# Kernel optimization log

Measured on AMD Instinct MI355X. Metric: run time of the kernel, lower is better.

Reference implementation:

```python
import jax, jax.numpy as jnp
import numpy as np

N_NODES = 50000
N_EDGES = 800000
IN_DIM = 128
HID = 32
HEADS = 4
OUT_DIM = 64
NEG_SLOPE = 0.2


def _glorot(key, shape):
    fan = shape[0] + shape[-1] if len(shape) > 1 else shape[-1]
    lim = jnp.sqrt(6.0 / fan)
    return jax.random.uniform(key, shape, jnp.float32, -lim, lim)


def setup_inputs() -> dict:
    key = jax.random.key(0)
    ks = jax.random.split(key, 10)
    x = jax.random.normal(ks[0], (N_NODES, IN_DIM), jnp.float32)
    edge_index = jax.random.randint(ks[1], (2, N_EDGES), 0, N_NODES, jnp.int32)
    # layer 1: in=IN_DIM, heads=HEADS, out=HID, concat
    W1 = _glorot(ks[2], (IN_DIM, HEADS * HID))
    a_src1 = _glorot(ks[3], (HEADS, HID))
    a_dst1 = _glorot(ks[4], (HEADS, HID))
    b1 = jnp.zeros((HEADS * HID,), jnp.float32)
    # layer 2: in=HEADS*HID, heads=1, out=OUT_DIM, mean
    W2 = _glorot(ks[5], (HEADS * HID, OUT_DIM))
    a_src2 = _glorot(ks[6], (1, OUT_DIM))
    a_dst2 = _glorot(ks[7], (1, OUT_DIM))
    b2 = jnp.zeros((OUT_DIM,), jnp.float32)
    return {"x": x, "edge_index": edge_index, "W1": W1, "a_src1": a_src1,
            "a_dst1": a_dst1, "b1": b1, "W2": W2, "a_src2": a_src2,
            "a_dst2": a_dst2, "b2": b2}


def gat_conv(x, src, dst, W, a_src, a_dst, bias, heads, out_ch, concat, num_nodes):
    # x: [N, in]; src/dst: [E] (self-loops already included)
    h = (x @ W).reshape(num_nodes, heads, out_ch)          # [N, H, F]
    alpha_s = jnp.einsum('nhf,hf->nh', h, a_src)           # [N, H]
    alpha_d = jnp.einsum('nhf,hf->nh', h, a_dst)
    e = alpha_s[src] + alpha_d[dst]                        # [E, H]
    e = jnp.where(e >= 0, e, NEG_SLOPE * e)                # leaky relu
    # segment softmax over destination neighborhoods
    e_max = jax.ops.segment_max(e, dst, num_segments=num_nodes)
    ex = jnp.exp(e - e_max[dst])
    denom = jax.ops.segment_sum(ex, dst, num_segments=num_nodes)
    alpha = ex / (denom[dst] + 1e-16)                      # [E, H]
    msg = h[src] * alpha[:, :, None]                       # [E, H, F]
    out = jax.ops.segment_sum(msg, dst, num_segments=num_nodes)  # [N, H, F]
    if concat:
        out = out.reshape(num_nodes, heads * out_ch)
    else:
        out = out.mean(axis=1)
    return out + bias


def reference(x, edge_index, W1, a_src1, a_dst1, b1, W2, a_src2, a_dst2, b2):
    n = x.shape[0]
    # PyG GATConv default add_self_loops=True
    loop = jnp.arange(n, dtype=edge_index.dtype)
    src = jnp.concatenate([edge_index[0], loop])
    dst = jnp.concatenate([edge_index[1], loop])
    h = gat_conv(x, src, dst, W1, a_src1, a_dst1, b1, HEADS, HID, True, n)
    h = jax.nn.relu(h)
    out = gat_conv(h, src, dst, W2, a_src2, a_dst2, b2, 1, OUT_DIM, False, n)
    return out
```

## Files before the change

### kernel.cpp

```cpp
#include <hip/hip_runtime.h>
#include <hip/hip_fp16.h>
#include <math.h>


#define NEG_SLOPE 0.2f
#define CAP 64

__device__ __forceinline__ float lrelu_exp(float e) {
    e = (e >= 0.f) ? e : NEG_SLOPE * e;
    return __expf(e);
}

__global__ __launch_bounds__(256) void build_kernel(
    const float* __restrict__ x, const float* __restrict__ W1,
    const float* __restrict__ a_src1, const float* __restrict__ a_dst1,
    __half* __restrict__ h1h, float* __restrict__ as1, float* __restrict__ ad1,
    const int* __restrict__ src, const int* __restrict__ dst,
    int* __restrict__ deg, unsigned short* __restrict__ col,
    int N, int E, int Gg) {
    __shared__ float Ws[32 * 128];
    __shared__ float xs[64 * 32];
    const int tid = threadIdx.x;

    if (blockIdx.x >= Gg) {
        const int base = (blockIdx.x - Gg) * 2048 + tid * 8;
        int s[8], d[8];
        if (base + 8 <= E) {
            int4 a0 = *(const int4*)&src[base];
            int4 a1 = *(const int4*)&src[base + 4];
            int4 c0 = *(const int4*)&dst[base];
            int4 c1 = *(const int4*)&dst[base + 4];
            s[0]=a0.x; s[1]=a0.y; s[2]=a0.z; s[3]=a0.w;
            s[4]=a1.x; s[5]=a1.y; s[6]=a1.z; s[7]=a1.w;
            d[0]=c0.x; d[1]=c0.y; d[2]=c0.z; d[3]=c0.w;
            d[4]=c1.x; d[5]=c1.y; d[6]=c1.z; d[7]=c1.w;
        } else {
#pragma unroll
            for (int u = 0; u < 8; ++u) {
                int i = base + u;
                if (i < E) { s[u] = src[i]; d[u] = dst[i]; }
                else       { s[u] = -1;     d[u] = -1; }
            }
        }
        int p[8];
#pragma unroll
        for (int u = 0; u < 8; ++u)
            if (d[u] >= 0) p[u] = atomicAdd(&deg[d[u]], 1);
#pragma unroll
        for (int u = 0; u < 8; ++u)
            if (d[u] >= 0 && p[u] < CAP)
                col[d[u] * CAP + p[u]] = (unsigned short)s[u];
        return;
    }

    const int tf = tid & 31;
    const int tn = tid >> 5;
    const int nb = blockIdx.x * 64;
    float acc[8][4];
#pragma unroll
    for (int i = 0; i < 8; ++i)
#pragma unroll
        for (int j = 0; j < 4; ++j) acc[i][j] = 0.f;

    for (int kc = 0; kc < 128; kc += 32) {
#pragma unroll
        for (int l = 0; l < 4; ++l) {
            int idx = tid + l * 256;
            int k = idx >> 5, f4 = idx & 31;
            *(float4*)&Ws[k * 128 + f4 * 4] =
                *(const float4*)&W1[(kc + k) * 128 + f4 * 4];
        }
#pragma unroll
        for (int l = 0; l < 2; ++l) {
            int idx = tid + l * 256;
            int n = idx >> 3, j = idx & 7;
            int gn = nb + n; if (gn >= N) gn = N - 1;
            *(float4*)&xs[n * 32 + j * 4] =
                *(const float4*)&x[gn * 128 + kc + j * 4];
        }
        __syncthreads();
#pragma unroll
        for (int k = 0; k < 32; ++k) {
            float4 w = *(const float4*)&Ws[k * 128 + tf * 4];
#pragma unroll
            for (int i = 0; i < 8; ++i) {
                float xv = xs[(tn * 8 + i) * 32 + k];
                acc[i][0] += xv * w.x; acc[i][1] += xv * w.y;
                acc[i][2] += xv * w.z; acc[i][3] += xv * w.w;
            }
        }
        __syncthreads();
    }
    float4 asv = *(const float4*)&a_src1[tf * 4];
    float4 adv = *(const float4*)&a_dst1[tf * 4];
    const int head = tf >> 3;
    const int lane8 = tf & 7;
#pragma unroll
    for (int i = 0; i < 8; ++i) {
        int n = nb + tn * 8 + i;
        if (n < N) {
            __half2 p0 = __floats2half2_rn(acc[i][0], acc[i][1]);
            __half2 p1 = __floats2half2_rn(acc[i][2], acc[i][3]);
            uint2 pk;
            pk.x = *(unsigned*)&p0;
            pk.y = *(unsigned*)&p1;
            *(uint2*)&h1h[(size_t)n * 128 + tf * 4] = pk;
        }
        float s = acc[i][0]*asv.x + acc[i][1]*asv.y + acc[i][2]*asv.z + acc[i][3]*asv.w;
        float d = acc[i][0]*adv.x + acc[i][1]*adv.y + acc[i][2]*adv.z + acc[i][3]*adv.w;
        s += __shfl_down(s, 4); d += __shfl_down(d, 4);
        s += __shfl_down(s, 2); d += __shfl_down(d, 2);
        s += __shfl_down(s, 1); d += __shfl_down(d, 1);
        if (lane8 == 0 && n < N) { as1[n * 4 + head] = s; ad1[n * 4 + head] = d; }
    }
}

__global__ __launch_bounds__(256) void agg1mm_kernel(
    const __half2* __restrict__ h1h2, const float* __restrict__ as1,
    const float* __restrict__ ad1, const float* __restrict__ b1,
    const float* __restrict__ W2, const float* __restrict__ a_src2,
    const float* __restrict__ a_dst2, const int* __restrict__ deg,
    const unsigned short* __restrict__ col,
    __half* __restrict__ h2h, float* __restrict__ as2, float* __restrict__ ad2,
    int N) {
    __shared__ float wls[4][4][68];
    __shared__ int   cls[4][64];
    __shared__ float hrs[4][128];
    __shared__ float part[16][64];
    const int tid = threadIdx.x;
    const int w = tid >> 6;
    const int lane = tid & 63;
    const int d = blockIdx.x * 4 + w;

    if (d < N) {
        const int hsel = lane >> 4;
        const float4 ad4 = *(const float4*)&ad1[4 * d];
        const float4 asd = *(const float4*)&as1[4 * d];
        const float adh = (hsel == 0) ? ad4.x : (hsel == 1) ? ad4.y
                        : (hsel == 2) ? ad4.z : ad4.w;
        const float ash = (hsel == 0) ? asd.x : (hsel == 1) ? asd.y
                        : (hsel == 2) ? asd.z : asd.w;
        const int dg = min(deg[d], CAP);
        const int dgp = (dg + 15) & ~15;
        const int beg = d * CAP;

        if (lane < dgp) {
            if (lane < dg) {
                int s = (int)col[beg + lane];
                cls[w][lane] = s;
                float4 a4 = *(const float4*)&as1[4 * s];
                wls[w][0][lane] = lrelu_exp(a4.x + ad4.x);
                wls[w][1][lane] = lrelu_exp(a4.y + ad4.y);
                wls[w][2][lane] = lrelu_exp(a4.z + ad4.z);
                wls[w][3][lane] = lrelu_exp(a4.w + ad4.w);
            } else {
                cls[w][lane] = 0;
                wls[w][0][lane] = 0.f;
                wls[w][1][lane] = 0.f;
                wls[w][2][lane] = 0.f;
                wls[w][3][lane] = 0.f;
            }
        }

        float wself = lrelu_exp(ash + adh);
        float2 vself = __half22float2(h1h2[((unsigned)d << 6) | (unsigned)lane]);
        float den = wself, accx = wself * vself.x, accy = wself * vself.y;

        for (int jj = 0; jj < dgp; jj += 16) {
            int4 c0 = *(const int4*)&cls[w][jj];
            int4 c1 = *(const int4*)&cls[w][jj + 4];
            int4 c2 = *(const int4*)&cls[w][jj + 8];
            int4 c3 = *(const int4*)&cls[w][jj + 12];
            int ss[16] = {c0.x, c0.y, c0.z, c0.w, c1.x, c1.y, c1.z, c1.w,
                          c2.x, c2.y, c2.z, c2.w, c3.x, c3.y, c3.z, c3.w};
            __half2 v[16];
#pragma unroll
            for (int u = 0; u < 16; ++u)
                v[u] = h1h2[(((unsigned)ss[u]) << 6) | (unsigned)lane];
            float4 w0 = *(const float4*)&wls[w][hsel][jj];
            float4 w1 = *(const float4*)&wls[w][hsel][jj + 4];
            float4 w2 = *(const float4*)&wls[w][hsel][jj + 8];
            float4 w3 = *(const float4*)&wls[w][hsel][jj + 12];
            float wt[16] = {w0.x, w0.y, w0.z, w0.w, w1.x, w1.y, w1.z, w1.w,
                            w2.x, w2.y, w2.z, w2.w, w3.x, w3.y, w3.z, w3.w};
#pragma unroll
            for (int u = 0; u < 16; ++u) {
                float2 vf = __half22float2(v[u]);
                den += wt[u];
                accx += wt[u] * vf.x;
                accy += wt[u] * vf.y;
            }
        }
        const float inv = 1.f / (den + 1e-16f);
        float2 bv = *(const float2*)&b1[lane * 2];
        float2 o;
        o.x = fmaxf(accx * inv + bv.x, 0.f);
        o.y = fmaxf(accy * inv + bv.y, 0.f);
        *(float2*)&hrs[w][lane * 2] = o;
    } else {
        hrs[w][lane * 2] = 0.f;
        hrs[w][lane * 2 + 1] = 0.f;
    }
    __syncthreads();

    float p0 = 0.f, p1 = 0.f, p2 = 0.f, p3 = 0.f;
#pragma unroll
    for (int kk = 0; kk < 32; kk += 4) {
        const int k = w * 32 + kk;
        float4 h0 = *(const float4*)&hrs[0][k];
        float4 h1 = *(const float4*)&hrs[1][k];
        float4 h2 = *(const float4*)&hrs[2][k];
        float4 h3 = *(const float4*)&hrs[3][k];
        float wv0 = W2[(k + 0) * 64 + lane];
        float wv1 = W2[(k + 1) * 64 + lane];
        float wv2 = W2[(k + 2) * 64 + lane];
        float wv3 = W2[(k + 3) * 64 + lane];
        p0 += h0.x * wv0 + h0.y * wv1 + h0.z * wv2 + h0.w * wv3;
        p1 += h1.x * wv0 + h1.y * wv1 + h1.z * wv2 + h1.w * wv3;
        p2 += h2.x * wv0 + h2.y * wv1 + h2.z * wv2 + h2.w * wv3;
        p3 += h3.x * wv0 + h3.y * wv1 + h3.z * wv2 + h3.w * wv3;
    }
    part[w * 4 + 0][lane] = p0;
    part[w * 4 + 1][lane] = p1;
    part[w * 4 + 2][lane] = p2;
    part[w * 4 + 3][lane] = p3;
    __syncthreads();

    if (d < N) {
        float h2f = part[0 * 4 + w][lane] + part[1 * 4 + w][lane] +
                    part[2 * 4 + w][lane] + part[3 * 4 + w][lane];
        h2h[((unsigned)d << 6) | (unsigned)lane] = __float2half(h2f);
        float s = h2f * a_src2[lane];
        float dv = h2f * a_dst2[lane];
        s += __shfl_down(s, 32); dv += __shfl_down(dv, 32);
        s += __shfl_down(s, 16); dv += __shfl_down(dv, 16);
        s += __shfl_down(s, 8);  dv += __shfl_down(dv, 8);
        s += __shfl_down(s, 4);  dv += __shfl_down(dv, 4);
        s += __shfl_down(s, 2);  dv += __shfl_down(dv, 2);
        s += __shfl_down(s, 1);  dv += __shfl_down(dv, 1);
        if (lane == 0) { as2[d] = s; ad2[d] = dv; }
    }
}

__global__ __launch_bounds__(256) void agg2_kernel(
    const __half* __restrict__ h2h, const float* __restrict__ as2,
    const float* __restrict__ ad2, const float* __restrict__ b2,
    const int* __restrict__ deg, const unsigned short* __restrict__ col,
    float* __restrict__ out, int N) {
    __shared__ int   cls[4][64];
    __shared__ float wl[4][64];
    const int lane = threadIdx.x & 63;
    const int w = threadIdx.x >> 6;
    const int d = blockIdx.x * 4 + w;
    if (d >= N) return;
    const int dg = min(deg[d], CAP);
    const int dgp = (dg + 15) & ~15;
    const int beg = d * CAP;
    const float adv = ad2[d];

    float wself = lrelu_exp(as2[d] + adv);
    float den = wself;
    float acc = wself * __half2float(h2h[((unsigned)d << 6) | (unsigned)lane]);

    if (lane < dgp) {
        if (lane < dg) {
            int s = (int)col[beg + lane];
            cls[w][lane] = s;
            wl[w][lane] = lrelu_exp(as2[s] + adv);
        } else {
            cls[w][lane] = 0;
            wl[w][lane] = 0.f;
        }
    }

    for (int jj = 0; jj < dgp; jj += 16) {
        int4 c0 = *(const int4*)&cls[w][jj];
        int4 c1 = *(const int4*)&cls[w][jj + 4];
        int4 c2 = *(const int4*)&cls[w][jj + 8];
        int4 c3 = *(const int4*)&cls[w][jj + 12];
        int ss[16] = {c0.x, c0.y, c0.z, c0.w, c1.x, c1.y, c1.z, c1.w,
                      c2.x, c2.y, c2.z, c2.w, c3.x, c3.y, c3.z, c3.w};
        __half v[16];
#pragma unroll
        for (int u = 0; u < 16; ++u)
            v[u] = h2h[(((unsigned)ss[u]) << 6) | (unsigned)lane];
        float4 w0 = *(const float4*)&wl[w][jj];
        float4 w1 = *(const float4*)&wl[w][jj + 4];
        float4 w2 = *(const float4*)&wl[w][jj + 8];
        float4 w3 = *(const float4*)&wl[w][jj + 12];
        float wt[16] = {w0.x, w0.y, w0.z, w0.w, w1.x, w1.y, w1.z, w1.w,
                        w2.x, w2.y, w2.z, w2.w, w3.x, w3.y, w3.z, w3.w};
#pragma unroll
        for (int u = 0; u < 16; ++u) {
            den += wt[u];
            acc += wt[u] * __half2float(v[u]);
        }
    }
    out[(size_t)d * 64 + lane] = acc / (den + 1e-16f) + b2[lane];
}

extern "C" void kernel_launch(void* const* d_in, const int* in_sizes, int n_in,
                              void* d_out, int out_size, void* d_ws, size_t ws_size,
                              hipStream_t stream) {
    const float* x      = (const float*)d_in[0];
    const int*   eidx   = (const int*)d_in[1];
    const float* W1     = (const float*)d_in[2];
    const float* a_src1 = (const float*)d_in[3];
    const float* a_dst1 = (const float*)d_in[4];
    const float* b1     = (const float*)d_in[5];
    const float* W2     = (const float*)d_in[6];
    const float* a_src2 = (const float*)d_in[7];
    const float* a_dst2 = (const float*)d_in[8];
    const float* b2     = (const float*)d_in[9];
    float* out = (float*)d_out;

    const int N = in_sizes[0] / 128;
    const int E = in_sizes[1] / 2;

    const int* src = eidx;
    const int* dst = eidx + E;

    float* ws_f = (float*)d_ws;
    float* as1 = ws_f;
    float* ad1 = as1 + (size_t)N * 4;
    float* as2 = ad1 + (size_t)N * 4;
    float* ad2 = as2 + (size_t)N;
    __half* h1h = (__half*)(ad2 + (size_t)N);
    __half* h2h = h1h + (size_t)N * 128;
    int* deg = (int*)(h2h + (size_t)N * 64);
    unsigned short* col = (unsigned short*)(deg + N);

    const int Gg = (N + 63) / 64;
    const int Gs = (E + 2047) / 2048;

    hipMemsetAsync(deg, 0, (size_t)N * sizeof(int), stream);

    build_kernel<<<Gg + Gs, 256, 0, stream>>>(x, W1, a_src1, a_dst1,
                                              h1h, as1, ad1,
                                              src, dst, deg, col, N, E, Gg);

    agg1mm_kernel<<<(N + 3) / 4, 256, 0, stream>>>(
        (const __half2*)h1h, as1, ad1, b1, W2, a_src2, a_dst2,
        deg, col, h2h, as2, ad2, N);

    agg2_kernel<<<(N + 3) / 4, 256, 0, stream>>>(h2h, as2, ad2, b2,
                                                 deg, col, out, N);
}
```

Before: 203.2 us.

## Compute layer-1 projection with fp16 MFMA instead of scalar FP32 FMA

Replaces the shared-memory tiled FP32 GEMM in the build kernel with MFMA 16x16x32 f16 instructions. W1 fragments are loaded directly from global memory into registers, and x rows are converted to fp16 on the fly. Results are staged through a padded half-precision shared tile so that h1h can be written with coalesced 16-byte stores and the attention logits computed per row and head. This also adds a launch-bounds occupancy hint. The trade-off is extra precision loss from rounding x and W1 to fp16 and strided uncached-style W1 loads per wave.

```diff
diff --git a/kernel.cpp b/kernel.cpp
--- a/kernel.cpp
+++ b/kernel.cpp
@@ -6,20 +6,22 @@
 #define NEG_SLOPE 0.2f
 #define CAP 64
 
+typedef _Float16 f16x8 __attribute__((ext_vector_type(8)));
+typedef float    f32x4 __attribute__((ext_vector_type(4)));
+
 __device__ __forceinline__ float lrelu_exp(float e) {
     e = (e >= 0.f) ? e : NEG_SLOPE * e;
     return __expf(e);
 }
 
-__global__ __launch_bounds__(256) void build_kernel(
+__global__ __launch_bounds__(256, 4) void build_kernel(
     const float* __restrict__ x, const float* __restrict__ W1,
     const float* __restrict__ a_src1, const float* __restrict__ a_dst1,
     __half* __restrict__ h1h, float* __restrict__ as1, float* __restrict__ ad1,
     const int* __restrict__ src, const int* __restrict__ dst,
     int* __restrict__ deg, unsigned short* __restrict__ col,
     int N, int E, int Gg) {
-    __shared__ float Ws[32 * 128];
-    __shared__ float xs[64 * 32];
+    __shared__ __half hs[64 * 136];
     const int tid = threadIdx.x;
 
     if (blockIdx.x >= Gg) {
@@ -53,65 +55,102 @@
         return;
     }
 
-    const int tf = tid & 31;
-    const int tn = tid >> 5;
-    const int nb = blockIdx.x * 64;
-    float acc[8][4];
-#pragma unroll
-    for (int i = 0; i < 8; ++i)
-#pragma unroll
-        for (int j = 0; j < 4; ++j) acc[i][j] = 0.f;
-
-    for (int kc = 0; kc < 128; kc += 32) {
-#pragma unroll
-        for (int l = 0; l < 4; ++l) {
-            int idx = tid + l * 256;
-            int k = idx >> 5, f4 = idx & 31;
-            *(float4*)&Ws[k * 128 + f4 * 4] =
-                *(const float4*)&W1[(kc + k) * 128 + f4 * 4];
-        }
-#pragma unroll
-        for (int l = 0; l < 2; ++l) {
-            int idx = tid + l * 256;
-            int n = idx >> 3, j = idx & 7;
-            int gn = nb + n; if (gn >= N) gn = N - 1;
-            *(float4*)&xs[n * 32 + j * 4] =
-                *(const float4*)&x[gn * 128 + kc + j * 4];
-        }
-        __syncthreads();
-#pragma unroll
-        for (int k = 0; k < 32; ++k) {
-            float4 w = *(const float4*)&Ws[k * 128 + tf * 4];
-#pragma unroll
-            for (int i = 0; i < 8; ++i) {
-                float xv = xs[(tn * 8 + i) * 32 + k];
-                acc[i][0] += xv * w.x; acc[i][1] += xv * w.y;
-                acc[i][2] += xv * w.z; acc[i][3] += xv * w.w;
-            }
-        }
-        __syncthreads();
-    }
-    float4 asv = *(const float4*)&a_src1[tf * 4];
-    float4 adv = *(const float4*)&a_dst1[tf * 4];
-    const int head = tf >> 3;
-    const int lane8 = tf & 7;
-#pragma unroll
-    for (int i = 0; i < 8; ++i) {
-        int n = nb + tn * 8 + i;
-        if (n < N) {
-            __half2 p0 = __floats2half2_rn(acc[i][0], acc[i][1]);
-            __half2 p1 = __floats2half2_rn(acc[i][2], acc[i][3]);
-            uint2 pk;
-            pk.x = *(unsigned*)&p0;
-            pk.y = *(unsigned*)&p1;
-            *(uint2*)&h1h[(size_t)n * 128 + tf * 4] = pk;
-        }
-        float s = acc[i][0]*asv.x + acc[i][1]*asv.y + acc[i][2]*asv.z + acc[i][3]*asv.w;
-        float d = acc[i][0]*adv.x + acc[i][1]*adv.y + acc[i][2]*adv.z + acc[i][3]*adv.w;
-        s += __shfl_down(s, 4); d += __shfl_down(d, 4);
-        s += __shfl_down(s, 2); d += __shfl_down(d, 2);
-        s += __shfl_down(s, 1); d += __shfl_down(d, 1);
-        if (lane8 == 0 && n < N) { as1[n * 4 + head] = s; ad1[n * 4 + head] = d; }
+    const int w    = tid >> 6;
+    const int lane = tid & 63;
+    const int r16  = lane & 15;
+    const int g4   = lane >> 4;
+    const int nb   = blockIdx.x * 64;
+
+    f16x8 bf[2][4];
+#pragma unroll
+    for (int ct = 0; ct < 2; ++ct) {
+        const int c = w * 32 + ct * 16 + r16;
+#pragma unroll
+        for (int ks = 0; ks < 4; ++ks) {
+            const float* wp = W1 + (size_t)(ks * 32 + g4 * 8) * 128 + c;
+            f16x8 b;
+#pragma unroll
+            for (int j = 0; j < 8; ++j)
+                b[j] = (_Float16)wp[(size_t)j * 128];
+            bf[ct][ks] = b;
+        }
+    }
+
+    f32x4 acc[4][2];
+#pragma unroll
+    for (int rt = 0; rt < 4; ++rt)
+#pragma unroll
+        for (int ct = 0; ct < 2; ++ct)
+            acc[rt][ct] = (f32x4){0.f, 0.f, 0.f, 0.f};
+
+#pragma unroll
+    for (int rt = 0; rt < 4; ++rt) {
+        int gr = nb + rt * 16 + r16;
+        if (gr >= N) gr = N - 1;
+        const float* xp = x + (size_t)gr * 128 + g4 * 8;
+        f16x8 af[4];
+#pragma unroll
+        for (int ks = 0; ks < 4; ++ks) {
+            float4 u0 = *(const float4*)(xp + ks * 32);
+            float4 u1 = *(const float4*)(xp + ks * 32 + 4);
+            f16x8 a;
+            a[0] = (_Float16)u0.x; a[1] = (_Float16)u0.y;
+            a[2] = (_Float16)u0.z; a[3] = (_Float16)u0.w;
+            a[4] = (_Float16)u1.x; a[5] = (_Float16)u1.y;
+            a[6] = (_Float16)u1.z; a[7] = (_Float16)u1.w;
+            af[ks] = a;
+        }
+#pragma unroll
+        for (int ct = 0; ct < 2; ++ct)
+#pragma unroll
+            for (int ks = 0; ks < 4; ++ks)
+                acc[rt][ct] = __builtin_amdgcn_mfma_f32_16x16x32_f16(
+                    af[ks], bf[ct][ks], acc[rt][ct], 0, 0, 0);
+    }
+
+#pragma unroll
+    for (int rt = 0; rt < 4; ++rt)
+#pragma unroll
+        for (int ct = 0; ct < 2; ++ct) {
+            const int c = w * 32 + ct * 16 + r16;
+#pragma unroll
+            for (int i = 0; i < 4; ++i) {
+                const int r = rt * 16 + g4 * 4 + i;
+                hs[r * 136 + c] = __float2half(acc[rt][ct][i]);
+            }
+        }
+    __syncthreads();
+
+#pragma unroll
+    for (int p = 0; p < 4; ++p) {
+        const int idx = tid + p * 256;
+        const int row = idx >> 4;
+        const int c8  = (idx & 15) << 3;
+        const int gn  = nb + row;
+        if (gn < N)
+            *(uint4*)&h1h[(size_t)gn * 128 + c8] =
+                *(const uint4*)&hs[row * 136 + c8];
+    }
+
+    {
+        const int row  = tid >> 2;
+        const int head = tid & 3;
+        const int gn   = nb + row;
+        if (gn < N) {
+            const __half* hp = &hs[row * 136 + head * 32];
+            float s = 0.f, dv = 0.f;
+#pragma unroll
+            for (int f4 = 0; f4 < 8; ++f4) {
+                float4 av = *(const float4*)&a_src1[head * 32 + f4 * 4];
+                float4 bv = *(const float4*)&a_dst1[head * 32 + f4 * 4];
+                float2 h01 = __half22float2(*(const __half2*)&hp[f4 * 4]);
+                float2 h23 = __half22float2(*(const __half2*)&hp[f4 * 4 + 2]);
+                s  += h01.x * av.x + h01.y * av.y + h23.x * av.z + h23.y * av.w;
+                dv += h01.x * bv.x + h01.y * bv.y + h23.x * bv.z + h23.y * bv.w;
+            }
+            as1[(size_t)gn * 4 + head] = s;
+            ad1[(size_t)gn * 4 + head] = dv;
+        }
     }
 }
 
```

Result: slower. 213.7 us (+5.2%).
